# Performance work log

Measured on AMD Instinct MI355X. Metric: run time of the kernel, lower is better.

The kernel has to match this reference:

```python
import jax, jax.numpy as jnp
import numpy as np

HIDDEN = 768
KEY = 128
SCALE = KEY ** (-0.5)


def _rope(x, pos):
    # pos: (1, L, KEY); first half is sin freqs, second half is cos (per torch code)
    half = pos.shape[-1] // 2
    sin = pos[..., :half]
    cos = pos[..., half:]
    x1 = x[..., :half]
    x2 = x[..., half:2 * half]
    return jnp.concatenate([x1 * cos - x2 * sin, x2 * cos + x1 * sin], axis=-1)


def setup_inputs() -> dict:
    key = jax.random.key(0)
    k1, k2, k3, k4 = jax.random.split(key, 4)
    B, L = 8, 2048
    x = jax.random.normal(k1, (B, L, HIDDEN // 2), dtype=jnp.float32)
    pos_emb = jax.random.normal(k2, (1, L, KEY * 2), dtype=jnp.float32)
    W_uv = jax.random.normal(k3, (HIDDEN // 2, 2 * HIDDEN + 2 * KEY), dtype=jnp.float32) * (HIDDEN // 2) ** (-0.5)
    W_out = jax.random.normal(k4, (HIDDEN, HIDDEN // 2), dtype=jnp.float32) * HIDDEN ** (-0.5)
    return {"x": x, "pos_emb": pos_emb, "W_uv": W_uv, "W_out": W_out}


def reference(x, pos_emb, W_uv, W_out):
    B, L, _ = x.shape
    uvqk = x @ W_uv  # (B, L, 2*HIDDEN + 2*KEY)
    u = uvqk[..., :HIDDEN]
    v = uvqk[..., HIDDEN:2 * HIDDEN]
    q = uvqk[..., 2 * HIDDEN:2 * HIDDEN + KEY]
    k = uvqk[..., 2 * HIDDEN + KEY:]
    u = jax.nn.silu(u)
    v = jax.nn.silu(v)
    pe = pos_emb[:, :L, :KEY]
    q = _rope(q, pe)
    k = _rope(k, pe)
    qk = jnp.einsum('bld,bmd->blm', q, k) * SCALE  # (B, L, L)
    attn = jax.nn.softmax(qk, axis=-1)
    out = jnp.einsum('blm,bmd->bld', attn, v)  # (B, L, HIDDEN)
    out = u * out
    return out @ W_out  # (B, L, HIDDEN//2)
```

## Files before the change

kernel.cpp:

```cpp
#include <hip/hip_runtime.h>
#include <hip/hip_bf16.h>
#include <math.h>

#define B_    8
#define L_    2048
#define HID   768
#define D2    384
#define NUV   1792
#define R_    16384
#define SCALE 0.08838834764831845f

typedef __attribute__((ext_vector_type(8))) short bf16x8;
typedef __attribute__((ext_vector_type(4))) float f32x4;
typedef unsigned int uint32;
typedef unsigned short ushort;

static __device__ __forceinline__ uint32 bfr(float x) {
    uint32 u = __float_as_uint(x);
    return (u + 0x7FFFu + ((u >> 16) & 1u)) >> 16;
}
static __device__ __forceinline__ uint32 pk2(float lo, float hi) {
    return bfr(lo) | (bfr(hi) << 16);
}
static __device__ __forceinline__ float bf2f(ushort u) {
    return __uint_as_float(((uint32)u) << 16);
}
static __device__ __forceinline__ float silu_f(float x) { return x / (1.0f + __expf(-x)); }

__global__ __launch_bounds__(256) void conv_all(
    const float* __restrict__ Wuv, ushort* __restrict__ WuvThi, ushort* __restrict__ WuvTlo,
    const float* __restrict__ Wout, ushort* __restrict__ WoutThi, ushort* __restrict__ WoutTlo,
    const float* __restrict__ X, ushort* __restrict__ Xhi)
{
    const int N1 = D2 * NUV;
    const int N2 = HID * D2;
    const int N3 = (R_ * D2) / 4;
    int idx = blockIdx.x * 256 + threadIdx.x;

    if (idx < N1) {
        int n = idx / D2, k = idx - n * D2;
        float v = Wuv[(size_t)k * NUV + n];
        uint32 h = bfr(v);
        WuvThi[idx] = (ushort)h;
        WuvTlo[idx] = (ushort)bfr(v - __uint_as_float(h << 16));
        return;
    }
    idx -= N1;
    if (idx < N2) {
        int n = idx / HID, k = idx - n * HID;
        float v = Wout[(size_t)k * D2 + n];
        uint32 h = bfr(v);
        WoutThi[idx] = (ushort)h;
        WoutTlo[idx] = (ushort)bfr(v - __uint_as_float(h << 16));
        return;
    }
    idx -= N2;
    if (idx < N3) {
        float4 v = *(const float4*)(X + (size_t)idx * 4);
        uint2 p; p.x = pk2(v.x, v.y); p.y = pk2(v.z, v.w);
        *(uint2*)(Xhi + (size_t)idx * 4) = p;
    }
}

template<int EPI>
__global__ __launch_bounds__(512, 4) void gemm_2p(
    const ushort* __restrict__ Ahi, int lda,
    const ushort* __restrict__ BThi, const ushort* __restrict__ BTlo, int ldbt,
    float* __restrict__ C, int ldc,
    float* __restrict__ u_buf, ushort* __restrict__ qk, ushort* __restrict__ vT,
    int K)
{
    __shared__ unsigned char As[128 * 128];
    __shared__ unsigned char Bs[128 * 256];

    const int t  = threadIdx.x;
    const int w  = t >> 6;
    const int l  = t & 63;
    const int g  = l >> 4;
    const int li = l & 15;
    const int wr = w >> 1;
    const int wc = w & 1;
    const int m0 = blockIdx.y * 128;
    const int n0 = blockIdx.x * 128;

    f32x4 acc[2][4];
#pragma unroll
    for (int i = 0; i < 2; ++i)
#pragma unroll
        for (int j = 0; j < 4; ++j) acc[i][j] = (f32x4){0.f, 0.f, 0.f, 0.f};

    for (int k0 = 0; k0 < K; k0 += 64) {
#pragma unroll
        for (int i = 0; i < 2; ++i) {
            int idx = t + i * 512;
            int row = idx >> 3;
            int c8  = idx & 7;
            uint4 v = *(const uint4*)(Ahi + (size_t)(m0 + row) * lda + k0 + c8 * 8);
            *(uint4*)&As[row * 128 + ((c8 * 16) ^ ((row & 7) << 4))] = v;
        }
#pragma unroll
        for (int i = 0; i < 8; ++i) {
            int idx = t + i * 512;
            int c   = idx >> 5;
            int s8  = idx & 31;
            const ushort* src = (s8 < 16)
                ? (BThi + (long long)(n0 + c) * ldbt + k0 + s8 * 4)
                : (BTlo + (long long)(n0 + c) * ldbt + k0 + (s8 - 16) * 4);
            *(uint2*)&Bs[c * 256 + ((s8 * 8) ^ ((c & 7) << 4))] = *(const uint2*)src;
        }
        __syncthreads();

#pragma unroll
        for (int ks = 0; ks < 2; ++ks) {
            bf16x8 ah[2], bh[4], bl[4];
#pragma unroll
            for (int mi = 0; mi < 2; ++mi) {
                int row = wr * 32 + mi * 16 + li;
                ah[mi] = *(const bf16x8*)&As[row * 128 + ((ks * 64 + g * 16) ^ ((row & 7) << 4))];
            }
#pragma unroll
            for (int ni = 0; ni < 4; ++ni) {
                int col = wc * 64 + ni * 16 + li;
                int off = (ks * 64 + g * 16) ^ ((col & 7) << 4);
                bh[ni] = *(const bf16x8*)&Bs[col * 256 + off];
                bl[ni] = *(const bf16x8*)&Bs[col * 256 + 128 + off];
            }
#pragma unroll
            for (int mi = 0; mi < 2; ++mi)
#pragma unroll
                for (int ni = 0; ni < 4; ++ni) {
                    acc[mi][ni] = __builtin_amdgcn_mfma_f32_16x16x32_bf16(ah[mi], bh[ni], acc[mi][ni], 0, 0, 0);
                    acc[mi][ni] = __builtin_amdgcn_mfma_f32_16x16x32_bf16(ah[mi], bl[ni], acc[mi][ni], 0, 0, 0);
                }
        }
        __syncthreads();
    }

    if (EPI == 0) {
#pragma unroll
        for (int mi = 0; mi < 2; ++mi)
#pragma unroll
            for (int ni = 0; ni < 4; ++ni) {
                int col = n0 + wc * 64 + ni * 16 + li;
#pragma unroll
                for (int r = 0; r < 4; ++r) {
                    int row = m0 + wr * 32 + mi * 16 + g * 4 + r;
                    C[(long long)row * ldc + col] = acc[mi][ni][r];
                }
            }
    } else {
        if (n0 < 768) {
#pragma unroll
            for (int mi = 0; mi < 2; ++mi)
#pragma unroll
                for (int ni = 0; ni < 4; ++ni) {
                    int col = n0 + wc * 64 + ni * 16 + li;
#pragma unroll
                    for (int r = 0; r < 4; ++r) {
                        int row = m0 + wr * 32 + mi * 16 + g * 4 + r;
                        u_buf[(long long)row * 768 + col] = silu_f(acc[mi][ni][r]);
                    }
                }
        } else if (n0 < 1536) {
            int bb = m0 >> 11;
            int llb = (m0 & 2047) + wr * 32 + g * 4;
#pragma unroll
            for (int mi = 0; mi < 2; ++mi) {
                int ll = llb + mi * 16;
#pragma unroll
                for (int ni = 0; ni < 4; ++ni) {
                    int cv = n0 + wc * 64 + ni * 16 + li - 768;
                    ushort* vb = vT + ((size_t)bb * 768 + cv) * 2048 + ll;
                    *(uint32*)(vb)     = pk2(silu_f(acc[mi][ni][0]), silu_f(acc[mi][ni][1]));
                    *(uint32*)(vb + 2) = pk2(silu_f(acc[mi][ni][2]), silu_f(acc[mi][ni][3]));
                }
            }
        } else {
#pragma unroll
            for (int mi = 0; mi < 2; ++mi)
#pragma unroll
                for (int ni = 0; ni < 4; ++ni) {
                    int qcol = n0 + wc * 64 + ni * 16 + li - 1536;
#pragma unroll
                    for (int r = 0; r < 4; ++r) {
                        int row = m0 + wr * 32 + mi * 16 + g * 4 + r;
                        qk[(size_t)row * 256 + qcol] = (ushort)bfr(acc[mi][ni][r]);
                    }
                }
        }
    }
}

__global__ __launch_bounds__(128) void rope_bf(ushort* __restrict__ qk,
                                               const float* __restrict__ pos)
{
    int row = blockIdx.x;
    int lpos = row & (L_ - 1);
    int t = threadIdx.x;
    int j = t & 63;
    int isK = t >> 6;
    ushort* base = qk + (size_t)row * 256 + isK * 128;
    float s = pos[lpos * 256 + j];
    float c = pos[lpos * 256 + 64 + j];
    float x1 = bf2f(base[j]);
    float x2 = bf2f(base[64 + j]);
    base[j]      = (ushort)bfr(x1 * c - x2 * s);
    base[64 + j] = (ushort)bfr(x2 * c + x1 * s);
}

__global__ __launch_bounds__(512) void fused_attn13(
    const float* __restrict__ u_buf, const ushort* __restrict__ qk,
    const ushort* __restrict__ vT, ushort* __restrict__ gated)
{
    __shared__ unsigned char KbB[128 * 256];
    __shared__ unsigned char PbB[64 * 256];
    __shared__ float lred[2][64];

    const int t  = threadIdx.x;
    const int w  = t >> 6;
    const int l  = t & 63;
    const int g  = l >> 4;
    const int li = l & 15;

    const int b  = blockIdx.x & 7;
    const int qt = blockIdx.x >> 3;
    const long long rowQ0 = (long long)b * L_ + (long long)qt * 64;
    const long long rowB0 = (long long)b * L_;

    const int rtq = w >> 1;
    const int ch  = w & 1;

    bf16x8 qf[4];
    {
        const ushort* qrow = qk + (rowQ0 + rtq * 16 + li) * 256;
#pragma unroll
        for (int ks = 0; ks < 4; ++ks)
            qf[ks] = *(const bf16x8*)&qrow[ks * 32 + g * 8];
    }

    float l_part[4] = {0.f, 0.f, 0.f, 0.f};

    f32x4 o[4][6];
#pragma unroll
    for (int rt = 0; rt < 4; ++rt)
#pragma unroll
        for (int ct = 0; ct < 6; ++ct)
            o[rt][ct] = (f32x4){0.f, 0.f, 0.f, 0.f};

    const ushort* vrow = vT + ((size_t)b * 768 + w * 96 + li) * 2048 + g * 8;

    const int kr  = t >> 4;
    const int c16 = t & 15;
    const int ksw = (c16 * 16) ^ ((kr & 7) << 4);

    uint4 kA = *(const uint4*)&qk[(rowB0 + kr)      * 256 + 128 + c16 * 8];
    uint4 kB = *(const uint4*)&qk[(rowB0 + kr + 32) * 256 + 128 + c16 * 8];
    uint4 kC = *(const uint4*)&qk[(rowB0 + kr + 64) * 256 + 128 + c16 * 8];
    uint4 kD = *(const uint4*)&qk[(rowB0 + kr + 96) * 256 + 128 + c16 * 8];

    union U16 { uint4 u; bf16x8 bv; };

    for (int jt = 0; jt < 16; ++jt) {
        *(uint4*)&KbB[(kr)      * 256 + ksw] = kA;
        *(uint4*)&KbB[(kr + 32) * 256 + ksw] = kB;
        *(uint4*)&KbB[(kr + 64) * 256 + ksw] = kC;
        *(uint4*)&KbB[(kr + 96) * 256 + ksw] = kD;
        __syncthreads();

        if (jt + 1 < 16) {
            const ushort* kn = qk + (rowB0 + (jt + 1) * 128) * 256 + 128 + c16 * 8;
            kA = *(const uint4*)(kn + (size_t)(kr)      * 256);
            kB = *(const uint4*)(kn + (size_t)(kr + 32) * 256);
            kC = *(const uint4*)(kn + (size_t)(kr + 64) * 256);
            kD = *(const uint4*)(kn + (size_t)(kr + 96) * 256);
        }

#pragma unroll
        for (int ci = 0; ci < 4; ++ci) {
            const int ct = ch * 4 + ci;
            const int krow = ct * 16 + li;
            const int rs = (krow & 7) << 4;
            f32x4 s = {0.f, 0.f, 0.f, 0.f};
#pragma unroll
            for (int ks = 0; ks < 4; ++ks) {
                bf16x8 kf = *(const bf16x8*)&KbB[krow * 256 + ((ks * 64 + g * 16) ^ rs)];
                s = __builtin_amdgcn_mfma_f32_16x16x32_bf16(qf[ks], kf, s, 0, 0, 0);
            }
#pragma unroll
            for (int r = 0; r < 4; ++r) {
                float p = __expf(SCALE * s[r]);
                l_part[r] += p;
                const int prow = rtq * 16 + g * 4 + r;
                *(ushort*)&PbB[prow * 256 + (((ct * 16 + li) * 2) ^ ((prow & 7) << 4))]
                    = (ushort)bfr(p);
            }
        }
        __syncthreads();

        const ushort* vj = vrow + jt * 128;
#pragma unroll
        for (int ks = 0; ks < 4; ++ks) {
            bf16x8 pa0 = *(const bf16x8*)&PbB[(0 * 16 + li) * 256 + ((ks * 64 + g * 16) ^ ((li & 7) << 4))];
            bf16x8 pa1 = *(const bf16x8*)&PbB[(1 * 16 + li) * 256 + ((ks * 64 + g * 16) ^ ((li & 7) << 4))];
            bf16x8 pa2 = *(const bf16x8*)&PbB[(2 * 16 + li) * 256 + ((ks * 64 + g * 16) ^ ((li & 7) << 4))];
            bf16x8 pa3 = *(const bf16x8*)&PbB[(3 * 16 + li) * 256 + ((ks * 64 + g * 16) ^ ((li & 7) << 4))];
            U16 vc0, vc1, vc2, vc3, vc4, vc5;
            vc0.u = *(const uint4*)(vj + (size_t)(0 * 16) * 2048 + ks * 32);
            vc1.u = *(const uint4*)(vj + (size_t)(1 * 16) * 2048 + ks * 32);
            vc2.u = *(const uint4*)(vj + (size_t)(2 * 16) * 2048 + ks * 32);
            vc3.u = *(const uint4*)(vj + (size_t)(3 * 16) * 2048 + ks * 32);
            vc4.u = *(const uint4*)(vj + (size_t)(4 * 16) * 2048 + ks * 32);
            vc5.u = *(const uint4*)(vj + (size_t)(5 * 16) * 2048 + ks * 32);
#define PV_CT(CT, VC) \
            o[0][CT] = __builtin_amdgcn_mfma_f32_16x16x32_bf16(pa0, VC.bv, o[0][CT], 0, 0, 0); \
            o[1][CT] = __builtin_amdgcn_mfma_f32_16x16x32_bf16(pa1, VC.bv, o[1][CT], 0, 0, 0); \
            o[2][CT] = __builtin_amdgcn_mfma_f32_16x16x32_bf16(pa2, VC.bv, o[2][CT], 0, 0, 0); \
            o[3][CT] = __builtin_amdgcn_mfma_f32_16x16x32_bf16(pa3, VC.bv, o[3][CT], 0, 0, 0);
            PV_CT(0, vc0)
            PV_CT(1, vc1)
            PV_CT(2, vc2)
            PV_CT(3, vc3)
            PV_CT(4, vc4)
            PV_CT(5, vc5)
#undef PV_CT
        }
    }

#pragma unroll
    for (int r = 0; r < 4; ++r) {
#pragma unroll
        for (int off = 8; off >= 1; off >>= 1)
            l_part[r] += __shfl_xor(l_part[r], off);
    }
    if (li == 0) {
#pragma unroll
        for (int r = 0; r < 4; ++r)
            lred[ch][rtq * 16 + g * 4 + r] = l_part[r];
    }
    __syncthreads();

#pragma unroll
    for (int rt = 0; rt < 4; ++rt) {
#pragma unroll
        for (int r = 0; r < 4; ++r) {
            const int row = rt * 16 + g * 4 + r;
            float inv = 1.0f / (lred[0][row] + lred[1][row]);
            const float* ub = u_buf + (rowQ0 + row) * 768;
            ushort* gb = gated + (rowQ0 + row) * 768;
#pragma unroll
            for (int ct = 0; ct < 6; ++ct) {
                int col = w * 96 + ct * 16 + li;
                gb[col] = (ushort)bfr(o[rt][ct][r] * inv * ub[col]);
            }
        }
    }
}

extern "C" void kernel_launch(void* const* d_in, const int* in_sizes, int n_in,
                              void* d_out, int out_size, void* d_ws, size_t ws_size,
                              hipStream_t stream)
{
    const float* x    = (const float*)d_in[0];
    const float* pos  = (const float*)d_in[1];
    const float* Wuv  = (const float*)d_in[2];
    const float* Wout = (const float*)d_in[3];
    float* out = (float*)d_out;

    float*  u_buf = (float*)d_ws;
    ushort* qk    = (ushort*)(u_buf + (size_t)R_ * HID);
    ushort* vT    = qk + (size_t)R_ * 256;
    ushort* WuvThi  = vT + (size_t)B_ * HID * L_;
    ushort* WuvTlo  = WuvThi + (size_t)NUV * D2;
    ushort* WoutThi = WuvTlo + (size_t)NUV * D2;
    ushort* WoutTlo = WoutThi + (size_t)D2 * HID;
    ushort* gated   = WoutTlo + (size_t)D2 * HID;
    ushort* xhi     = gated;

    size_t need = ((size_t)R_ * HID) * 4 +
                  ((size_t)R_ * 256 + (size_t)B_ * HID * L_ +
                   2 * (size_t)NUV * D2 + 2 * (size_t)D2 * HID +
                   (size_t)R_ * HID) * 2;
    if (ws_size < need) return;

    {
        int total = D2 * NUV + HID * D2 + (R_ * D2) / 4;
        conv_all<<<dim3((total + 255) / 256), dim3(256), 0, stream>>>(
            Wuv, WuvThi, WuvTlo, Wout, WoutThi, WoutTlo, x, xhi);
    }

    gemm_2p<1><<<dim3(NUV / 128, R_ / 128), dim3(512), 0, stream>>>(
        xhi, D2, WuvThi, WuvTlo, D2, nullptr, 0, u_buf, qk, vT, D2);

    rope_bf<<<dim3(R_), dim3(128), 0, stream>>>(qk, pos);

    fused_attn13<<<dim3(256), dim3(512), 0, stream>>>(u_buf, qk, vT, gated);

    gemm_2p<0><<<dim3(D2 / 128, R_ / 128), dim3(512), 0, stream>>>(
        gated, HID, WoutThi, WoutTlo, HID, out, D2, nullptr, nullptr, nullptr, HID);
}
```

Before: 232.9 us.

## Double-buffer K and P tiles in attention, one barrier per iteration, add setprio

Splits the K and P shared-memory tiles into two buffers each. This drops the attention loop from two barriers per iteration to one, and the next K tile is written to LDS while the other buffer is in use. Global loads for the K tile two steps ahead are issued after the barrier. s_setprio hints are placed around the MFMA sections to favour matrix issue across waves. Shared memory grows to about 97KB per block, which could limit occupancy, although the 256-block grid already runs one block per CU.

```diff
diff --git a/kernel.cpp b/kernel.cpp
--- a/kernel.cpp
+++ b/kernel.cpp
@@ -208,12 +208,12 @@
     base[64 + j] = (ushort)bfr(x2 * c + x1 * s);
 }
 
-__global__ __launch_bounds__(512) void fused_attn13(
+__global__ __launch_bounds__(512) void fused_attn15(
     const float* __restrict__ u_buf, const ushort* __restrict__ qk,
     const ushort* __restrict__ vT, ushort* __restrict__ gated)
 {
-    __shared__ unsigned char KbB[128 * 256];
-    __shared__ unsigned char PbB[64 * 256];
+    __shared__ unsigned char KbB[2][128 * 256];
+    __shared__ unsigned char PbB[2][64 * 256];
     __shared__ float lred[2][64];
 
     const int t  = threadIdx.x;
@@ -253,28 +253,30 @@
     const int c16 = t & 15;
     const int ksw = (c16 * 16) ^ ((kr & 7) << 4);
 
+    union U16 { uint4 u; bf16x8 bv; };
+
     uint4 kA = *(const uint4*)&qk[(rowB0 + kr)      * 256 + 128 + c16 * 8];
     uint4 kB = *(const uint4*)&qk[(rowB0 + kr + 32) * 256 + 128 + c16 * 8];
     uint4 kC = *(const uint4*)&qk[(rowB0 + kr + 64) * 256 + 128 + c16 * 8];
     uint4 kD = *(const uint4*)&qk[(rowB0 + kr + 96) * 256 + 128 + c16 * 8];
-
-    union U16 { uint4 u; bf16x8 bv; };
+    *(uint4*)&KbB[0][(kr)      * 256 + ksw] = kA;
+    *(uint4*)&KbB[0][(kr + 32) * 256 + ksw] = kB;
+    *(uint4*)&KbB[0][(kr + 64) * 256 + ksw] = kC;
+    *(uint4*)&KbB[0][(kr + 96) * 256 + ksw] = kD;
+    __syncthreads();
+    {
+        const ushort* kn = qk + (rowB0 + 128 + kr) * 256 + 128 + c16 * 8;
+        kA = *(const uint4*)(kn);
+        kB = *(const uint4*)(kn + (size_t)32 * 256);
+        kC = *(const uint4*)(kn + (size_t)64 * 256);
+        kD = *(const uint4*)(kn + (size_t)96 * 256);
+    }
 
     for (int jt = 0; jt < 16; ++jt) {
-        *(uint4*)&KbB[(kr)      * 256 + ksw] = kA;
-        *(uint4*)&KbB[(kr + 32) * 256 + ksw] = kB;
-        *(uint4*)&KbB[(kr + 64) * 256 + ksw] = kC;
-        *(uint4*)&KbB[(kr + 96) * 256 + ksw] = kD;
-        __syncthreads();
-
-        if (jt + 1 < 16) {
-            const ushort* kn = qk + (rowB0 + (jt + 1) * 128) * 256 + 128 + c16 * 8;
-            kA = *(const uint4*)(kn + (size_t)(kr)      * 256);
-            kB = *(const uint4*)(kn + (size_t)(kr + 32) * 256);
-            kC = *(const uint4*)(kn + (size_t)(kr + 64) * 256);
-            kD = *(const uint4*)(kn + (size_t)(kr + 96) * 256);
-        }
-
+        const unsigned char* Kb = &KbB[jt & 1][0];
+        unsigned char* Pb = &PbB[jt & 1][0];
+
+        __builtin_amdgcn_s_setprio(1);
 #pragma unroll
         for (int ci = 0; ci < 4; ++ci) {
             const int ct = ch * 4 + ci;
@@ -283,7 +285,7 @@
             f32x4 s = {0.f, 0.f, 0.f, 0.f};
 #pragma unroll
             for (int ks = 0; ks < 4; ++ks) {
-                bf16x8 kf = *(const bf16x8*)&KbB[krow * 256 + ((ks * 64 + g * 16) ^ rs)];
+                bf16x8 kf = *(const bf16x8*)&Kb[krow * 256 + ((ks * 64 + g * 16) ^ rs)];
                 s = __builtin_amdgcn_mfma_f32_16x16x32_bf16(qf[ks], kf, s, 0, 0, 0);
             }
 #pragma unroll
@@ -291,19 +293,37 @@
                 float p = __expf(SCALE * s[r]);
                 l_part[r] += p;
                 const int prow = rtq * 16 + g * 4 + r;
-                *(ushort*)&PbB[prow * 256 + (((ct * 16 + li) * 2) ^ ((prow & 7) << 4))]
+                *(ushort*)&Pb[prow * 256 + (((ct * 16 + li) * 2) ^ ((prow & 7) << 4))]
                     = (ushort)bfr(p);
             }
         }
+        __builtin_amdgcn_s_setprio(0);
+
+        if (jt + 1 < 16) {
+            unsigned char* Kn = &KbB[(jt + 1) & 1][0];
+            *(uint4*)&Kn[(kr)      * 256 + ksw] = kA;
+            *(uint4*)&Kn[(kr + 32) * 256 + ksw] = kB;
+            *(uint4*)&Kn[(kr + 64) * 256 + ksw] = kC;
+            *(uint4*)&Kn[(kr + 96) * 256 + ksw] = kD;
+        }
+
         __syncthreads();
 
+        if (jt + 2 < 16) {
+            const ushort* kn = qk + (rowB0 + (jt + 2) * 128 + kr) * 256 + 128 + c16 * 8;
+            kA = *(const uint4*)(kn);
+            kB = *(const uint4*)(kn + (size_t)32 * 256);
+            kC = *(const uint4*)(kn + (size_t)64 * 256);
+            kD = *(const uint4*)(kn + (size_t)96 * 256);
+        }
+
         const ushort* vj = vrow + jt * 128;
 #pragma unroll
         for (int ks = 0; ks < 4; ++ks) {
-            bf16x8 pa0 = *(const bf16x8*)&PbB[(0 * 16 + li) * 256 + ((ks * 64 + g * 16) ^ ((li & 7) << 4))];
-            bf16x8 pa1 = *(const bf16x8*)&PbB[(1 * 16 + li) * 256 + ((ks * 64 + g * 16) ^ ((li & 7) << 4))];
-            bf16x8 pa2 = *(const bf16x8*)&PbB[(2 * 16 + li) * 256 + ((ks * 64 + g * 16) ^ ((li & 7) << 4))];
-            bf16x8 pa3 = *(const bf16x8*)&PbB[(3 * 16 + li) * 256 + ((ks * 64 + g * 16) ^ ((li & 7) << 4))];
+            bf16x8 pa0 = *(const bf16x8*)&Pb[(0 * 16 + li) * 256 + ((ks * 64 + g * 16) ^ ((li & 7) << 4))];
+            bf16x8 pa1 = *(const bf16x8*)&Pb[(1 * 16 + li) * 256 + ((ks * 64 + g * 16) ^ ((li & 7) << 4))];
+            bf16x8 pa2 = *(const bf16x8*)&Pb[(2 * 16 + li) * 256 + ((ks * 64 + g * 16) ^ ((li & 7) << 4))];
+            bf16x8 pa3 = *(const bf16x8*)&Pb[(3 * 16 + li) * 256 + ((ks * 64 + g * 16) ^ ((li & 7) << 4))];
             U16 vc0, vc1, vc2, vc3, vc4, vc5;
             vc0.u = *(const uint4*)(vj + (size_t)(0 * 16) * 2048 + ks * 32);
             vc1.u = *(const uint4*)(vj + (size_t)(1 * 16) * 2048 + ks * 32);
@@ -311,6 +331,7 @@
             vc3.u = *(const uint4*)(vj + (size_t)(3 * 16) * 2048 + ks * 32);
             vc4.u = *(const uint4*)(vj + (size_t)(4 * 16) * 2048 + ks * 32);
             vc5.u = *(const uint4*)(vj + (size_t)(5 * 16) * 2048 + ks * 32);
+            __builtin_amdgcn_s_setprio(1);
 #define PV_CT(CT, VC) \
             o[0][CT] = __builtin_amdgcn_mfma_f32_16x16x32_bf16(pa0, VC.bv, o[0][CT], 0, 0, 0); \
             o[1][CT] = __builtin_amdgcn_mfma_f32_16x16x32_bf16(pa1, VC.bv, o[1][CT], 0, 0, 0); \
@@ -323,6 +344,7 @@
             PV_CT(4, vc4)
             PV_CT(5, vc5)
 #undef PV_CT
+            __builtin_amdgcn_s_setprio(0);
         }
     }
 
@@ -393,7 +415,7 @@
 
     rope_bf<<<dim3(R_), dim3(128), 0, stream>>>(qk, pos);
 
-    fused_attn13<<<dim3(256), dim3(512), 0, stream>>>(u_buf, qk, vT, gated);
+    fused_attn15<<<dim3(256), dim3(512), 0, stream>>>(u_buf, qk, vT, gated);
 
     gemm_2p<0><<<dim3(D2 / 128, R_ / 128), dim3(512), 0, stream>>>(
         gated, HID, WoutThi, WoutTlo, HID, out, D2, nullptr, nullptr, nullptr, HID);
```

Measured after the change: 229.2 us. No clear change (-1.6%).
